# Optimization experiments

Measured on AMD Instinct MI355X. Metric: run time of the kernel, lower is better.

Reference implementation:

```python
import jax, jax.numpy as jnp
import numpy as np

B, T, D, H, DH, COUT, PRED, K, DFF = 16, 512, 512, 8, 64, 7, 96, 16, 2048
LOW_FREQ = 1
LN_EPS = 1e-5


def _next_fast_len(n):
    while True:
        m = n
        for p in (2, 3, 5):
            while m % p == 0:
                m //= p
        if m == 1:
            return n
        n += 1


def conv1d_fft(f, g, axis=1):
    # FFT cross-correlation, matching torch conv1d_fft (roll + tail slice)
    N = f.shape[axis]
    M = g.shape[axis]
    L = _next_fast_len(N + M - 1)
    Ff = jnp.fft.rfft(f, n=L, axis=axis)
    Fg = jnp.fft.rfft(g, n=L, axis=axis)
    out = jnp.fft.irfft(Ff * jnp.conj(Fg), n=L, axis=axis)
    out = jnp.roll(out, -1, axis=axis)
    return jax.lax.slice_in_dim(out, L - N, L, axis=axis)


def es_weights(sw, T_):
    alpha = jax.nn.sigmoid(sw)                       # (h,1)
    powers = jnp.arange(T_, dtype=jnp.float32)       # (T,)
    init_w = alpha ** (powers + 1.0)                 # (h,T)
    w = (1.0 - alpha) * alpha ** powers[::-1]        # (h,T)
    return init_w.T[None, :, :, None], w.T[None, :, :, None]  # (1,T,h,1)


def exponential_smoothing(values, v0, sw, aux_values=None):
    b, t, h, d = values.shape
    init_w, w = es_weights(sw, t)
    out = init_w * v0 + conv1d_fft(values, w, axis=1)
    if aux_values is not None:
        alpha = jax.nn.sigmoid(sw).reshape(1, 1, h, 1)
        aux_w = w / jnp.maximum(1.0 - alpha, 1e-6) * alpha
        out = out + conv1d_fft(aux_values, aux_w, axis=1)
    return out


def fourier_extrapolate(x, pred_len, k, low_freq=LOW_FREQ):
    b, t, d = x.shape
    x_freq = jnp.fft.rfft(x, axis=1)                 # (b, t//2+1, d)
    hi_end = x_freq.shape[1] - 1 if t % 2 == 0 else x_freq.shape[1]
    x_freq_high = x_freq[:, low_freq:hi_end]
    k_ = k if (k is not None and k < t // 2) else max(1, hi_end - low_freq)
    k_ = min(k_, x_freq_high.shape[1])
    mag = jnp.abs(x_freq_high).transpose(0, 2, 1)    # (b,d,F)
    _, idx = jax.lax.top_k(mag, k_)                  # (b,d,k)
    idx = idx.transpose(0, 2, 1) + low_freq          # (b,k,d)
    x_topk = jnp.take_along_axis(x_freq, idx, axis=1)
    freqs = jnp.fft.rfftfreq(t).astype(jnp.float32)
    f_topk = jnp.take_along_axis(
        jnp.broadcast_to(freqs[None, :, None], (b, freqs.shape[0], d)), idx, axis=1)
    x_ex = jnp.concatenate([x_topk, jnp.conj(x_topk)], axis=1)   # (b,2k,d)
    f_ex = jnp.concatenate([f_topk, -f_topk], axis=1)
    tt = jnp.arange(t + pred_len, dtype=jnp.float32)[None, None, :, None]
    amp = (jnp.abs(x_ex) / t)[:, :, None, :]
    phase = jnp.angle(x_ex)[:, :, None, :]
    x_time = amp * jnp.cos(2.0 * jnp.pi * f_ex[:, :, None, :] * tt + phase)
    return x_time.sum(axis=1)                        # (b, t+pred_len, d)


def layer_norm(x, g, b, eps=LN_EPS):
    mu = x.mean(-1, keepdims=True)
    var = ((x - mu) ** 2).mean(-1, keepdims=True)
    return (x - mu) / jnp.sqrt(var + eps) * g + b


def _forward(res, level, Wi, bi, z0, v0_g, sw_g, Wo, bo, W1, W2,
             g1, b1_ln, g2, b2_ln, Wg, bg, Ws, bs, v0_l, sw_l):
    b, t, _ = res.shape
    # season block
    season = fourier_extrapolate(res, PRED, K)               # (b, t+PRED, d)
    res1 = res - season[:, :t]
    # growth block
    v = (res1 @ Wi.T + bi).reshape(b, t, H, DH)
    v = jnp.concatenate([jnp.broadcast_to(z0[None, None], (b, 1, H, DH)), v], axis=1)
    diffs = v[:, 1:] - v[:, :-1]                             # (b,t,H,DH)
    sm = exponential_smoothing(diffs, v0_g, sw_g)
    gr = jnp.concatenate([jnp.broadcast_to(v0_g, (b, 1, H, DH)), sm], axis=1)
    growth = gr.reshape(b, t + 1, H * DH) @ Wo.T + bo        # (b,t+1,d)
    # residual path
    h = layer_norm(res1 - growth[:, 1:], g1, b1_ln)
    ff = jax.nn.relu(h @ W1.T) @ W2.T
    h = layer_norm(h + ff, g2, b2_ln)
    # level block
    gp = growth[:, 1:t + 1] @ Wg.T + bg                      # (b,t,COUT)
    sp = season[:, :t] @ Ws.T + bs
    es_in = (level - sp)[..., None]                          # (b,t,COUT,1)
    lvl = exponential_smoothing(es_in, v0_l, sw_l, aux_values=gp[..., None])[..., 0]
    return h, lvl, growth, season


def setup_inputs() -> dict:
    key = jax.random.key(0)
    ks = jax.random.split(key, 20)
    s = 0.02
    return {
        "res": jax.random.normal(ks[0], (B, T, D), jnp.float32),
        "level": jax.random.normal(ks[1], (B, T, COUT), jnp.float32),
        "Wi": jax.random.normal(ks[2], (H * DH, D), jnp.float32) * s,
        "bi": jnp.zeros((H * DH,), jnp.float32),
        "z0": jax.random.normal(ks[3], (H, DH), jnp.float32),
        "v0_g": jax.random.normal(ks[4], (1, 1, H, DH), jnp.float32),
        "sw_g": jax.random.normal(ks[5], (H, 1), jnp.float32),
        "Wo": jax.random.normal(ks[6], (D, H * DH), jnp.float32) * s,
        "bo": jnp.zeros((D,), jnp.float32),
        "W1": jax.random.normal(ks[7], (DFF, D), jnp.float32) * s,
        "W2": jax.random.normal(ks[8], (D, DFF), jnp.float32) * s,
        "g1": jnp.ones((D,), jnp.float32),
        "b1_ln": jnp.zeros((D,), jnp.float32),
        "g2": jnp.ones((D,), jnp.float32),
        "b2_ln": jnp.zeros((D,), jnp.float32),
        "Wg": jax.random.normal(ks[9], (COUT, D), jnp.float32) * s,
        "bg": jnp.zeros((COUT,), jnp.float32),
        "Ws": jax.random.normal(ks[10], (COUT, D), jnp.float32) * s,
        "bs": jnp.zeros((COUT,), jnp.float32),
        "v0_l": jax.random.normal(ks[11], (1, 1, COUT, 1), jnp.float32),
        "sw_l": jax.random.normal(ks[12], (COUT, 1), jnp.float32),
    }


def reference(res, level, Wi, bi, z0, v0_g, sw_g, Wo, bo, W1, W2,
              g1, b1_ln, g2, b2_ln, Wg, bg, Ws, bs, v0_l, sw_l):
    return _forward(res, level, Wi, bi, z0, v0_g, sw_g, Wo, bo, W1, W2,
                    g1, b1_ln, g2, b2_ln, Wg, bg, Ws, bs, v0_l, sw_l)
```

## Files before the change

kernel.cpp:

```cpp
#include <hip/hip_runtime.h>
#include <math.h>

#define Bn 16
#define Tn 512
#define Dn 512
#define COUTn 7
#define PREDn 96

using f32x4 = __attribute__((ext_vector_type(4))) float;
using bf16x8 = __attribute__((ext_vector_type(8))) __bf16;

__device__ __forceinline__ unsigned short f2b(float f) {
  unsigned int u = __float_as_uint(f);
  u += 0x7fff + ((u >> 16) & 1);
  return (unsigned short)(u >> 16);
}

__device__ __forceinline__ void gld16(const void* g, void* l) {
  __builtin_amdgcn_global_load_lds(
      (const __attribute__((address_space(1))) void*)g,
      (__attribute__((address_space(3))) void*)l, 16, 0, 0);
}

__global__ __launch_bounds__(256) void cvt_bf16(
    const float* __restrict__ in, unsigned short* __restrict__ out, int n) {
  int i = (blockIdx.x * 256 + threadIdx.x) * 4;
  if (i + 3 < n) {
    float4 v = *reinterpret_cast<const float4*>(&in[i]);
    ushort4 o;
    o.x = f2b(v.x); o.y = f2b(v.y); o.z = f2b(v.z); o.w = f2b(v.w);
    *reinterpret_cast<ushort4*>(&out[i]) = o;
  }
}

__global__ __launch_bounds__(256) void twiddle_init2(
    unsigned short* __restrict__ twc_b, unsigned short* __restrict__ tws_b,
    double* __restrict__ tabw, float* __restrict__ c512,
    float* __restrict__ s512) {
  int idx = blockIdx.x * 256 + threadIdx.x;
  int k = idx >> 9, t = idx & 511;
  int m = (k * t) & 511;
  double ang = (double)m * (M_PI / 256.0);
  twc_b[idx] = f2b((float)cos(ang));
  tws_b[idx] = f2b((float)sin(ang));
  if (idx < 512) {
    double a2 = (double)idx * (M_PI / 256.0);
    c512[idx] = (float)cos(a2);
    s512[idx] = (float)sin(a2);
    tabw[2 * idx] = cos(a2);
    tabw[2 * idx + 1] = -sin(a2);
  }
}

__global__ __launch_bounds__(256) void transpose_cvt(
    const float* __restrict__ res, unsigned short* __restrict__ resT) {
  __shared__ unsigned short tile[64][65];
  int b = blockIdx.z;
  int t0 = blockIdx.y * 64, d0 = blockIdx.x * 64;
  int tid = threadIdx.x;
  int c = tid & 63, r4 = (tid >> 6) * 16;
#pragma unroll
  for (int i = 0; i < 16; ++i) {
    int t = t0 + r4 + i;
    tile[r4 + i][c] = f2b(res[((size_t)(b * 512 + t)) * 512 + d0 + c]);
  }
  __syncthreads();
#pragma unroll
  for (int i = 0; i < 16; ++i) {
    int d = d0 + r4 + i;
    resT[((size_t)(b * 512 + d)) * 512 + t0 + c] = tile[c][r4 + i];
  }
}

__global__ __launch_bounds__(256) void screen_mfma(
    const unsigned short* __restrict__ twc_b,
    const unsigned short* __restrict__ tws_b,
    const unsigned short* __restrict__ resT, float* __restrict__ mag) {
  __shared__ unsigned short lAc[2][2048];
  __shared__ unsigned short lAs[2][2048];
  __shared__ unsigned short lB[2][4096];
  int tid = threadIdx.x;
  int wv = tid >> 6, lane = tid & 63;
  int b = blockIdx.z;
  int k0 = blockIdx.y * 64;
  int d0 = blockIdx.x * 128;

  int rA = wv * 16 + (lane >> 2);
  int rB0 = wv * 32 + (lane >> 2);
  int rB1 = rB0 + 16;
  int kk = (lane & 3) * 8;
  int kkA = kk ^ (((rA >> 1) & 3) << 3);
  int kkB0 = kk ^ (((rB0 >> 1) & 3) << 3);
  int kkB1 = kk ^ (((rB1 >> 1) & 3) << 3);
  const unsigned short* ac = twc_b + (size_t)(k0 + rA) * 512 + kkA;
  const unsigned short* as = tws_b + (size_t)(k0 + rA) * 512 + kkA;
  const unsigned short* bb0 = resT + ((size_t)(b * 512 + d0 + rB0)) * 512 + kkB0;
  const unsigned short* bb1 = resT + ((size_t)(b * 512 + d0 + rB1)) * 512 + kkB1;

  int frow = lane & 15, fk = (lane >> 4) * 8;
  int ia[4], ib[2];
#pragma unroll
  for (int i = 0; i < 4; ++i) {
    int r = i * 16 + frow;
    ia[i] = r * 32 + (fk ^ (((r >> 1) & 3) << 3));
  }
#pragma unroll
  for (int j = 0; j < 2; ++j) {
    int r = wv * 32 + j * 16 + frow;
    ib[j] = r * 32 + (fk ^ (((r >> 1) & 3) << 3));
  }

  f32x4 accR[4][2] = {};
  f32x4 accI[4][2] = {};

  gld16(ac, &lAc[0][wv * 512]);
  gld16(as, &lAs[0][wv * 512]);
  gld16(bb0, &lB[0][wv * 1024]);
  gld16(bb1, &lB[0][wv * 1024 + 512]);
  __syncthreads();

  int cur = 0;
  for (int t = 0; t < 16; ++t) {
    if (t + 1 < 16) {
      int ko = (t + 1) * 32;
      gld16(ac + ko, &lAc[cur ^ 1][wv * 512]);
      gld16(as + ko, &lAs[cur ^ 1][wv * 512]);
      gld16(bb0 + ko, &lB[cur ^ 1][wv * 1024]);
      gld16(bb1 + ko, &lB[cur ^ 1][wv * 1024 + 512]);
    }
    bf16x8 afc[4], afs[4], bw[2];
#pragma unroll
    for (int i = 0; i < 4; ++i) {
      afc[i] = *reinterpret_cast<const bf16x8*>(&lAc[cur][ia[i]]);
      afs[i] = *reinterpret_cast<const bf16x8*>(&lAs[cur][ia[i]]);
    }
#pragma unroll
    for (int j = 0; j < 2; ++j)
      bw[j] = *reinterpret_cast<const bf16x8*>(&lB[cur][ib[j]]);
#pragma unroll
    for (int i = 0; i < 4; ++i)
#pragma unroll
      for (int j = 0; j < 2; ++j) {
        accR[i][j] = __builtin_amdgcn_mfma_f32_16x16x32_bf16(
            afc[i], bw[j], accR[i][j], 0, 0, 0);
        accI[i][j] = __builtin_amdgcn_mfma_f32_16x16x32_bf16(
            afs[i], bw[j], accI[i][j], 0, 0, 0);
      }
    __syncthreads();
    cur ^= 1;
  }

  int ccol = lane & 15, crow4 = (lane >> 4) * 4;
#pragma unroll
  for (int i = 0; i < 4; ++i) {
    int kb = k0 + i * 16 + crow4;
#pragma unroll
    for (int j = 0; j < 2; ++j) {
      int d = d0 + wv * 32 + j * 16 + ccol;
#pragma unroll
      for (int r = 0; r < 4; ++r) {
        float re = accR[i][j][r], im = accI[i][j][r];
        mag[((size_t)(b * 256 + kb + r)) * 512 + d] = re * re + im * im;
      }
    }
  }
}

__global__ __launch_bounds__(64) void cand32(
    const float* __restrict__ mag, int* __restrict__ cand) {
  int blk = blockIdx.x;
  int b = blk >> 9;
  int d = blk & 511;
  int lane = threadIdx.x;
  float m2[4];
#pragma unroll
  for (int i = 0; i < 4; ++i) {
    int k = 1 + lane + 64 * i;
    m2[i] = (k <= 255) ? mag[((size_t)(b * 256 + k)) * 512 + d] : -1.f;
  }
  for (int j = 0; j < 32; ++j) {
    float bm = -2.f; int bk = 1 << 20;
#pragma unroll
    for (int i = 0; i < 4; ++i) {
      int k = 1 + lane + 64 * i;
      if (m2[i] > bm || (m2[i] == bm && k < bk)) { bm = m2[i]; bk = k; }
    }
    for (int o = 32; o > 0; o >>= 1) {
      float om = __shfl_down(bm, o, 64);
      int ok = __shfl_down(bk, o, 64);
      if (om > bm || (om == bm && ok < bk)) { bm = om; bk = ok; }
    }
    bk = __shfl(bk, 0, 64);
    if (lane == 0) cand[((size_t)(b * 32 + j)) * 512 + d] = bk;
#pragma unroll
    for (int i = 0; i < 4; ++i) {
      int k = 1 + lane + 64 * i;
      if (k == bk) m2[i] = -1.f;
    }
  }
}

__global__ __launch_bounds__(512) void refine32(
    const float* __restrict__ res, const int* __restrict__ cand,
    const double* __restrict__ tabw, int* __restrict__ kidx,
    float* __restrict__ cjb, float* __restrict__ sjb) {
  int b = blockIdx.y;
  int d0 = blockIdx.x * 16;
  int tid = threadIdx.x;
  __shared__ float colbuf[512][17];
  for (int idx = tid; idx < 8192; idx += 512) {
    int t = idx >> 4, c = idx & 15;
    colbuf[t][c] = res[((size_t)(b * 512 + t)) * 512 + d0 + c];
  }
  __syncthreads();

  int j = tid & 31, c = tid >> 5;
  int k = cand[((size_t)(b * 32 + j)) * 512 + d0 + c];
  double wr = tabw[2 * k], wi = tabw[2 * k + 1];
  double zr = 1.0, zi = 0.0, ar = 0.0, ai = 0.0;
#pragma unroll 4
  for (int t = 0; t < 512; ++t) {
    double x = (double)colbuf[t][c];
    ar = fma(x, zr, ar);
    ai = fma(x, zi, ai);
    double nzr = fma(zr, wr, -zi * wi);
    double nzi = fma(zr, wi, zi * wr);
    zr = nzr; zi = nzi;
  }
  double m2 = ar * ar + ai * ai;
  float cjv = (float)(ar * (2.0 / 512.0));
  float sjv = (float)(ai * (2.0 / 512.0));
  for (int jo = 0; jo < 16; ++jo) {
    double bm = m2; int bk = k;
#pragma unroll
    for (int o = 16; o > 0; o >>= 1) {
      double om = __shfl_xor(bm, o, 32);
      int ok = __shfl_xor(bk, o, 32);
      if (om > bm || (om == bm && ok < bk)) { bm = om; bk = ok; }
    }
    if (k == bk) {
      size_t o = ((size_t)(b * 16 + jo)) * 512 + d0 + c;
      kidx[o] = k; cjb[o] = cjv; sjb[o] = sjv;
      m2 = -1.0;
    }
  }
}

__global__ __launch_bounds__(512) void synth_kernel(
    const int* __restrict__ kidx, const float* __restrict__ cjb,
    const float* __restrict__ sjb, const float* __restrict__ c512,
    const float* __restrict__ s512, const float* __restrict__ res,
    float* __restrict__ season, unsigned short* __restrict__ res1b) {
  int b = blockIdx.y;
  int t0 = blockIdx.x * 16;
  int d = threadIdx.x;

  __shared__ float ct[512], st[512];
  ct[d] = c512[d];
  st[d] = s512[d];
  __syncthreads();

  int kk[16];
  float cw[16], sw[16];
#pragma unroll
  for (int j = 0; j < 16; ++j) {
    size_t o = ((size_t)(b * 16 + j)) * 512 + d;
    kk[j] = kidx[o];
    cw[j] = cjb[o];
    sw[j] = sjb[o];
  }

  for (int tt = 0; tt < 16; ++tt) {
    int t = t0 + tt;
    if (t >= Tn + PREDn) break;
    float acc = 0.f;
#pragma unroll
    for (int j = 0; j < 16; ++j) {
      int m = (kk[j] * t) & 511;
      acc += cw[j] * ct[m] - sw[j] * st[m];
    }
    season[((size_t)(b * (Tn + PREDn) + t)) * 512 + d] = acc;
    if (t < Tn) {
      size_t o = ((size_t)(b * Tn + t)) * 512 + d;
      res1b[o] = f2b(res[o] - acc);
    }
  }
}

template <int MODE, int BN>
__global__ __launch_bounds__(256) void gemm_mfma(
    const unsigned short* __restrict__ A, const unsigned short* __restrict__ W,
    const float* __restrict__ bias, float* __restrict__ C,
    unsigned short* __restrict__ Cb, int M, int N, int Kd, int ldk) {
  constexpr int NF = BN / 32;
  __shared__ unsigned short lA[2][4096];
  __shared__ unsigned short lB[2][BN * 32];
  int tid = threadIdx.x;
  int wv = tid >> 6, lane = tid & 63;
  int m0 = blockIdx.y * 128, n0 = blockIdx.x * BN;
  int koff = blockIdx.z * Kd;
  int wr = (wv >> 1) * 64, wc = (wv & 1) * (BN / 2);

  int rA0 = wv * 32 + (lane >> 2);
  int rA1 = rA0 + 16;
  int kk = (lane & 3) * 8;
  int kkA0 = kk ^ (((rA0 >> 1) & 3) << 3);
  int kkA1 = kk ^ (((rA1 >> 1) & 3) << 3);
  int gmA0 = m0 + rA0; if (gmA0 > M - 1) gmA0 = M - 1;
  int gmA1 = m0 + rA1; if (gmA1 > M - 1) gmA1 = M - 1;
  const unsigned short* a0 = A + (size_t)gmA0 * ldk + koff + kkA0;
  const unsigned short* a1 = A + (size_t)gmA1 * ldk + koff + kkA1;

  const unsigned short* b0;
  const unsigned short* b1 = nullptr;
  int dBo;
  if constexpr (BN == 128) {
    int rB0 = wv * 32 + (lane >> 2);
    int rB1 = rB0 + 16;
    int kkB0 = kk ^ (((rB0 >> 1) & 3) << 3);
    int kkB1 = kk ^ (((rB1 >> 1) & 3) << 3);
    b0 = W + (size_t)(n0 + rB0) * ldk + koff + kkB0;
    b1 = W + (size_t)(n0 + rB1) * ldk + koff + kkB1;
    dBo = wv * 1024;
  } else {
    int rB = wv * 16 + (lane >> 2);
    int kkB = kk ^ (((rB >> 1) & 3) << 3);
    b0 = W + (size_t)(n0 + rB) * ldk + koff + kkB;
    dBo = wv * 512;
  }

  int frow = lane & 15, fk = (lane >> 4) * 8;
  int ia[4], ib[NF];
#pragma unroll
  for (int i = 0; i < 4; ++i) {
    int r = wr + i * 16 + frow;
    ia[i] = r * 32 + (fk ^ (((r >> 1) & 3) << 3));
  }
#pragma unroll
  for (int j = 0; j < NF; ++j) {
    int r = wc + j * 16 + frow;
    ib[j] = r * 32 + (fk ^ (((r >> 1) & 3) << 3));
  }

  f32x4 acc[4][NF] = {};
  int nk = Kd >> 5;

  gld16(a0, &lA[0][wv * 1024]);
  gld16(a1, &lA[0][wv * 1024 + 512]);
  gld16(b0, &lB[0][dBo]);
  if constexpr (BN == 128) gld16(b1, &lB[0][dBo + 512]);
  __syncthreads();

  int cur = 0;
  for (int t = 0; t < nk; ++t) {
    if (t + 1 < nk) {
      int ko = (t + 1) << 5;
      gld16(a0 + ko, &lA[cur ^ 1][wv * 1024]);
      gld16(a1 + ko, &lA[cur ^ 1][wv * 1024 + 512]);
      gld16(b0 + ko, &lB[cur ^ 1][dBo]);
      if constexpr (BN == 128) gld16(b1 + ko, &lB[cur ^ 1][dBo + 512]);
    }
    bf16x8 af[4], bw[NF];
#pragma unroll
    for (int i = 0; i < 4; ++i)
      af[i] = *reinterpret_cast<const bf16x8*>(&lA[cur][ia[i]]);
#pragma unroll
    for (int j = 0; j < NF; ++j)
      bw[j] = *reinterpret_cast<const bf16x8*>(&lB[cur][ib[j]]);
#pragma unroll
    for (int i = 0; i < 4; ++i)
#pragma unroll
      for (int j = 0; j < NF; ++j)
        acc[i][j] = __builtin_amdgcn_mfma_f32_16x16x32_bf16(
            af[i], bw[j], acc[i][j], 0, 0, 0);
    __syncthreads();
    cur ^= 1;
  }

  int ccol = lane & 15, crow4 = (lane >> 4) * 4;
#pragma unroll
  for (int i = 0; i < 4; ++i) {
    int gm0 = m0 + wr + i * 16 + crow4;
#pragma unroll
    for (int j = 0; j < NF; ++j) {
      int gn = n0 + wc + j * 16 + ccol;
      float bv = 0.f;
      if (MODE == 0) bv = bias[gn];
#pragma unroll
      for (int r = 0; r < 4; ++r) {
        int gm = gm0 + r;
        if (gm < M) {
          size_t o = (size_t)gm * N + gn;
          float v = acc[i][j][r] + bv;
          if (MODE == 1) Cb[o] = f2b(fmaxf(v, 0.f));
          else if (MODE == 3) atomicAdd(&C[o], v);
          else C[o] = v;
        }
      }
    }
  }
}

__global__ __launch_bounds__(256) void ema_gA(
    const float* __restrict__ v, const float* __restrict__ z0,
    const float* __restrict__ sw_g, float* __restrict__ tmp,
    float* __restrict__ sumend) {
  int g = blockIdx.x * 256 + threadIdx.x;
  int hd = g & 511;
  int ch = (g >> 9) & 7;
  int b = g >> 12;
  int h = hd >> 6;
  float alpha = 1.f / (1.f + expf(-sw_g[h]));
  float om = 1.f - alpha;
  int t0 = ch * 64;
  float prev = (t0 == 0) ? z0[hd] : v[((size_t)(b * 512 + t0 - 1)) * 512 + hd];
  float s = 0.f;
  for (int i = 0; i < 64; ++i) {
    float cur = v[((size_t)(b * 512 + t0 + i)) * 512 + hd];
    s = alpha * s + om * (cur - prev);
    prev = cur;
    tmp[((size_t)(b * 512 + t0 + i)) * 512 + hd] = s;
  }
  sumend[((size_t)(b * 512 + hd)) * 8 + ch] = s;
}

__global__ __launch_bounds__(256) void ema_gB(
    const float* __restrict__ sumend, const float* __restrict__ v0_g,
    const float* __restrict__ sw_g, float* __restrict__ carry,
    unsigned short* __restrict__ grb) {
  int g = blockIdx.x * 256 + threadIdx.x;
  int hd = g & 511, b = g >> 9, h = hd >> 6;
  float alpha = 1.f / (1.f + expf(-sw_g[h]));
  float A64 = exp2f(64.f * log2f(alpha));
  float cin = v0_g[hd];
  grb[((size_t)(b * 513)) * 512 + hd] = f2b(cin);
  for (int ch = 0; ch < 8; ++ch) {
    carry[((size_t)(b * 512 + hd)) * 8 + ch] = cin;
    cin = A64 * cin + sumend[((size_t)(b * 512 + hd)) * 8 + ch];
  }
}

__global__ __launch_bounds__(256) void ema_gC(
    const float* __restrict__ tmp, const float* __restrict__ carry,
    const float* __restrict__ sw_g, unsigned short* __restrict__ grb) {
  int g = blockIdx.x * 256 + threadIdx.x;
  int hd = g & 511;
  int t = (g >> 9) & 511;
  int b = g >> 18;
  int h = hd >> 6;
  float alpha = 1.f / (1.f + expf(-sw_g[h]));
  int ch = t >> 6, i = t & 63;
  float Ai = exp2f((float)(i + 1) * log2f(alpha));
  float s = tmp[g] + Ai * carry[((size_t)(b * 512 + hd)) * 8 + ch];
  grb[((size_t)(b * 513 + t + 1)) * 512 + hd] = f2b(s);
}

__global__ __launch_bounds__(256) void ln0_kernel(
    const float* __restrict__ res, const float* __restrict__ season,
    const float* __restrict__ growth, const float* __restrict__ g,
    const float* __restrict__ bvec, float* __restrict__ h1,
    unsigned short* __restrict__ h1b) {
  int row = blockIdx.x, b = row >> 9, t = row & 511;
  int tid = threadIdx.x;
  const float* xr = res + (size_t)row * 512;
  const float* sr = season + ((size_t)(b * (Tn + PREDn) + t)) * 512;
  const float* gr = growth + ((size_t)(b * (Tn + 1) + t + 1)) * 512;
  float2 xv = *reinterpret_cast<const float2*>(&xr[tid * 2]);
  float2 sv = *reinterpret_cast<const float2*>(&sr[tid * 2]);
  float2 gv2 = *reinterpret_cast<const float2*>(&gr[tid * 2]);
  float v0 = xv.x - sv.x - gv2.x;
  float v1 = xv.y - sv.y - gv2.y;
  float s1 = v0 + v1;
  float s2 = v0 * v0 + v1 * v1;
  for (int o = 32; o > 0; o >>= 1) {
    s1 += __shfl_down(s1, o, 64);
    s2 += __shfl_down(s2, o, 64);
  }
  __shared__ float r1[4], r2[4];
  __shared__ float mu_s, rstd_s;
  int wv = tid >> 6, ln = tid & 63;
  if (ln == 0) { r1[wv] = s1; r2[wv] = s2; }
  __syncthreads();
  if (tid == 0) {
    float S1 = r1[0] + r1[1] + r1[2] + r1[3];
    float S2 = r2[0] + r2[1] + r2[2] + r2[3];
    float mu = S1 * (1.0f / 512.0f);
    float var = S2 * (1.0f / 512.0f) - mu * mu;
    mu_s = mu;
    rstd_s = rsqrtf(var + 1e-5f);
  }
  __syncthreads();
  float mu = mu_s, rstd = rstd_s;
  float2 gv = *reinterpret_cast<const float2*>(&g[tid * 2]);
  float2 bv = *reinterpret_cast<const float2*>(&bvec[tid * 2]);
  float o0 = (v0 - mu) * rstd * gv.x + bv.x;
  float o1 = (v1 - mu) * rstd * gv.y + bv.y;
  size_t o = (size_t)row * 512 + tid * 2;
  *reinterpret_cast<float2*>(&h1[o]) = make_float2(o0, o1);
  ushort2 hb; hb.x = f2b(o0); hb.y = f2b(o1);
  *reinterpret_cast<ushort2*>(&h1b[o]) = hb;
}

__global__ __launch_bounds__(256) void ln1_kernel(
    const float* __restrict__ X, const float* __restrict__ g,
    const float* __restrict__ bvec, float* __restrict__ out) {
  int row = blockIdx.x;
  int tid = threadIdx.x;
  const float* xr = X + (size_t)row * 512;
  float2 xv = *reinterpret_cast<const float2*>(&xr[tid * 2]);
  float v0 = xv.x, v1 = xv.y;
  float s1 = v0 + v1;
  float s2 = v0 * v0 + v1 * v1;
  for (int o = 32; o > 0; o >>= 1) {
    s1 += __shfl_down(s1, o, 64);
    s2 += __shfl_down(s2, o, 64);
  }
  __shared__ float r1[4], r2[4];
  __shared__ float mu_s, rstd_s;
  int wv = tid >> 6, ln = tid & 63;
  if (ln == 0) { r1[wv] = s1; r2[wv] = s2; }
  __syncthreads();
  if (tid == 0) {
    float S1 = r1[0] + r1[1] + r1[2] + r1[3];
    float S2 = r2[0] + r2[1] + r2[2] + r2[3];
    float mu = S1 * (1.0f / 512.0f);
    float var = S2 * (1.0f / 512.0f) - mu * mu;
    mu_s = mu;
    rstd_s = rsqrtf(var + 1e-5f);
  }
  __syncthreads();
  float mu = mu_s, rstd = rstd_s;
  float2 gv = *reinterpret_cast<const float2*>(&g[tid * 2]);
  float2 bv = *reinterpret_cast<const float2*>(&bvec[tid * 2]);
  float o0 = (v0 - mu) * rstd * gv.x + bv.x;
  float o1 = (v1 - mu) * rstd * gv.y + bv.y;
  *reinterpret_cast<float2*>(&out[(size_t)row * 512 + tid * 2]) =
      make_float2(o0, o1);
}

__global__ __launch_bounds__(64) void proj7_dual(
    const float* __restrict__ growth, const float* __restrict__ season,
    const float* __restrict__ Wg, const float* __restrict__ bg,
    const float* __restrict__ Wse, const float* __restrict__ bs,
    float* __restrict__ gpb, float* __restrict__ spb) {
  int bt = blockIdx.x;
  int which = blockIdx.y;
  int b = bt >> 9;
  int t = bt & 511;
  int lane = threadIdx.x;
  const float* X = which ? season : growth;
  int strB = which ? (Tn + PREDn) : (Tn + 1);
  int off = which ? 0 : 1;
  const float* Wc = which ? Wse : Wg;
  const float* bc = which ? bs : bg;
  float* outp = which ? spb : gpb;
  const float* row = X + ((size_t)(b * strB + off + t)) * 512;
  float x[8];
#pragma unroll
  for (int i = 0; i < 8; ++i) x[i] = row[lane + 64 * i];
#pragma unroll
  for (int c = 0; c < 7; ++c) {
    float s = 0.f;
#pragma unroll
    for (int i = 0; i < 8; ++i) s += x[i] * Wc[c * 512 + lane + 64 * i];
    for (int o = 32; o > 0; o >>= 1) s += __shfl_down(s, o, 64);
    if (lane == 0) outp[((size_t)bt) * 7 + c] = s + bc[c];
  }
}

__global__ __launch_bounds__(256) void lvl_scan(
    const float* __restrict__ level, const float* __restrict__ sp,
    const float* __restrict__ gp, const float* __restrict__ v0_l,
    const float* __restrict__ sw_l, float* __restrict__ out_lvl) {
  int blk = blockIdx.x;
  int b = blk / 7, c = blk % 7;
  int tid = threadIdx.x;
  float alpha = 1.f / (1.f + expf(-sw_l[c]));
  float om = 1.f - alpha;
  size_t i0 = ((size_t)(b * 512 + 2 * tid)) * 7 + c;
  size_t i1 = i0 + 7;
  float u0 = om * (level[i0] - sp[i0]) + alpha * gp[i0];
  float u1 = om * (level[i1] - sp[i1]) + alpha * gp[i1];
  __shared__ float As[256], Us[256];
  As[tid] = alpha * alpha;
  Us[tid] = alpha * u0 + u1;
  __syncthreads();
  for (int off = 1; off < 256; off <<= 1) {
    float Ap = 1.f, Up = 0.f;
    if (tid >= off) { Ap = As[tid - off]; Up = Us[tid - off]; }
    __syncthreads();
    if (tid >= off) {
      float Ac = As[tid], Uc = Us[tid];
      As[tid] = Ac * Ap;
      Us[tid] = Ac * Up + Uc;
    }
    __syncthreads();
  }
  float v0 = v0_l[c];
  float Aex = (tid == 0) ? 1.f : As[tid - 1];
  float Uex = (tid == 0) ? 0.f : Us[tid - 1];
  float sprev = Aex * v0 + Uex;
  float o0 = alpha * sprev + u0;
  float o1 = alpha * o0 + u1;
  out_lvl[i0] = o0;
  out_lvl[i1] = o1;
}

extern "C" void kernel_launch(void* const* d_in, const int* in_sizes, int n_in,
                              void* d_out, int out_size, void* d_ws,
                              size_t ws_size, hipStream_t stream) {
  const float* res = (const float*)d_in[0];
  const float* level = (const float*)d_in[1];
  const float* Wi = (const float*)d_in[2];
  const float* bi = (const float*)d_in[3];
  const float* z0 = (const float*)d_in[4];
  const float* v0_g = (const float*)d_in[5];
  const float* sw_g = (const float*)d_in[6];
  const float* Wo = (const float*)d_in[7];
  const float* bo = (const float*)d_in[8];
  const float* W1 = (const float*)d_in[9];
  const float* W2 = (const float*)d_in[10];
  const float* g1 = (const float*)d_in[11];
  const float* b1 = (const float*)d_in[12];
  const float* g2 = (const float*)d_in[13];
  const float* b2 = (const float*)d_in[14];
  const float* Wg = (const float*)d_in[15];
  const float* bg = (const float*)d_in[16];
  const float* Wse = (const float*)d_in[17];
  const float* bs = (const float*)d_in[18];
  const float* v0_l = (const float*)d_in[19];
  const float* sw_l = (const float*)d_in[20];

  float* out = (float*)d_out;
  float* out_h = out;
  float* out_lvl = out + 4194304;
  float* out_growth = out + 4251648;
  float* out_season = out + 8454144;

  float* wsf = (float*)d_ws;
  unsigned short* res1_b = (unsigned short*)wsf;
  unsigned short* h1_b = (unsigned short*)wsf;
  float* gpb = wsf;
  float* spb = wsf + 57344;
  unsigned short* resT_b = (unsigned short*)(wsf + 2097152);
  float* magb = wsf + 4194304;
  int* candb = (int*)(wsf + 6291456);
  unsigned short* twc_b = (unsigned short*)(wsf + 6553600);
  unsigned short* tws_b = (unsigned short*)(wsf + 6619136);
  float* vbuf = wsf + 2097152;
  unsigned short* grbuf_b = (unsigned short*)(wsf + 6291456);
  float* sumend = wsf + 8392704;
  float* carryb = wsf + 8458240;
  unsigned short* ff1_b = (unsigned short*)(wsf + 2097152);
  double* tabw = (double*)(wsf + 10485760);
  float* c512 = wsf + 10487808;
  float* s512 = wsf + 10488320;
  int* kidx = (int*)(wsf + 10488832);
  float* cjb = wsf + 10619904;
  float* sjb = wsf + 10750976;
  float* tmpb = wsf + 10485760;
  float* h1 = wsf + 10485760;
  unsigned short* Wi_b = (unsigned short*)(wsf + 14680064);
  unsigned short* Wo_b = (unsigned short*)(wsf + 14811136);
  unsigned short* W1_b = (unsigned short*)(wsf + 14942208);
  unsigned short* W2_b = (unsigned short*)(wsf + 15466496);

  hipLaunchKernelGGL(cvt_bf16, dim3(256), dim3(256), 0, stream, Wi, Wi_b, 262144);
  hipLaunchKernelGGL(cvt_bf16, dim3(256), dim3(256), 0, stream, Wo, Wo_b, 262144);
  hipLaunchKernelGGL(cvt_bf16, dim3(1024), dim3(256), 0, stream, W1, W1_b, 1048576);
  hipLaunchKernelGGL(cvt_bf16, dim3(1024), dim3(256), 0, stream, W2, W2_b, 1048576);

  hipLaunchKernelGGL(twiddle_init2, dim3(512), dim3(256), 0, stream,
                     twc_b, tws_b, tabw, c512, s512);
  hipLaunchKernelGGL(transpose_cvt, dim3(8, 8, 16), dim3(256), 0, stream,
                     res, resT_b);
  hipLaunchKernelGGL(screen_mfma, dim3(4, 4, 16), dim3(256), 0, stream,
                     twc_b, tws_b, resT_b, magb);
  hipLaunchKernelGGL(cand32, dim3(8192), dim3(64), 0, stream, magb, candb);
  hipLaunchKernelGGL(refine32, dim3(32, 16), dim3(512), 0, stream,
                     res, candb, tabw, kidx, cjb, sjb);
  hipLaunchKernelGGL(synth_kernel, dim3(38, 16), dim3(512), 0, stream,
                     kidx, cjb, sjb, c512, s512, res, out_season, res1_b);
  hipLaunchKernelGGL((gemm_mfma<0, 64>), dim3(8, 64, 1), dim3(256), 0, stream,
                     res1_b, Wi_b, bi, vbuf, (unsigned short*)nullptr,
                     8192, 512, 512, 512);
  hipLaunchKernelGGL(ema_gA, dim3(256), dim3(256), 0, stream,
                     vbuf, z0, sw_g, tmpb, sumend);
  hipLaunchKernelGGL(ema_gB, dim3(32), dim3(256), 0, stream,
                     sumend, v0_g, sw_g, carryb, grbuf_b);
  hipLaunchKernelGGL(ema_gC, dim3(16384), dim3(256), 0, stream,
                     tmpb, carryb, sw_g, grbuf_b);
  hipLaunchKernelGGL((gemm_mfma<0, 64>), dim3(8, 65, 1), dim3(256), 0, stream,
                     grbuf_b, Wo_b, bo, out_growth, (unsigned short*)nullptr,
                     8208, 512, 512, 512);
  hipLaunchKernelGGL(ln0_kernel, dim3(Bn * Tn), dim3(256), 0, stream,
                     res, out_season, out_growth, g1, b1, h1, h1_b);
  hipLaunchKernelGGL((gemm_mfma<1, 128>), dim3(16, 64, 1), dim3(256), 0, stream,
                     h1_b, W1_b, (const float*)nullptr, (float*)nullptr, ff1_b,
                     8192, 2048, 512, 512);
  hipLaunchKernelGGL((gemm_mfma<3, 64>), dim3(8, 64, 4), dim3(256), 0, stream,
                     ff1_b, W2_b, (const float*)nullptr, h1,
                     (unsigned short*)nullptr, 8192, 512, 512, 2048);
  hipLaunchKernelGGL(ln1_kernel, dim3(Bn * Tn), dim3(256), 0, stream,
                     h1, g2, b2, out_h);
  hipLaunchKernelGGL(proj7_dual, dim3(Bn * Tn, 2), dim3(64), 0, stream,
                     out_growth, out_season, Wg, bg, Wse, bs, gpb, spb);
  hipLaunchKernelGGL(lvl_scan, dim3(112), dim3(256), 0, stream,
                     level, spb, gpb, v0_l, sw_l, out_lvl);

  (void)in_sizes; (void)n_in; (void)out_size; (void)ws_size;
}
```

Measured before the change: 506.9 us.

## Generalize GEMM tiles to 64x128, swap grid axes, replace split-K atomics with two passes

The MFMA GEMM is templated on both tile dimensions and all four projections now use 64x128 tiles. The grid is reordered so blockIdx.x walks M, which changes how blocks share weight tiles in cache. The FFN down-projection drops the 4-way split-K with atomicAdd and instead runs two sequential launches over K halves that add into the residual with plain read-modify-write. This removes atomic traffic but adds a launch, halves the parallelism of the W2 GEMM, and changes tile occupancy for every GEMM.

Result: faster. 481.4 us (-5.0%).

```diff
diff --git a/kernel.cpp b/kernel.cpp
--- a/kernel.cpp
+++ b/kernel.cpp
@@ -287,52 +287,44 @@
   }
 }
 
-template <int MODE, int BN>
+template <int MODE, int BM, int BN>
 __global__ __launch_bounds__(256) void gemm_mfma(
     const unsigned short* __restrict__ A, const unsigned short* __restrict__ W,
     const float* __restrict__ bias, float* __restrict__ C,
-    unsigned short* __restrict__ Cb, int M, int N, int Kd, int ldk) {
+    unsigned short* __restrict__ Cb, int M, int N, int Kd, int ldk,
+    int k0off) {
+  constexpr int MF = BM / 32;
   constexpr int NF = BN / 32;
-  __shared__ unsigned short lA[2][4096];
+  constexpr int NSA = BM / 64;
+  constexpr int NSB = BN / 64;
+  __shared__ unsigned short lA[2][BM * 32];
   __shared__ unsigned short lB[2][BN * 32];
   int tid = threadIdx.x;
   int wv = tid >> 6, lane = tid & 63;
-  int m0 = blockIdx.y * 128, n0 = blockIdx.x * BN;
-  int koff = blockIdx.z * Kd;
-  int wr = (wv >> 1) * 64, wc = (wv & 1) * (BN / 2);
-
-  int rA0 = wv * 32 + (lane >> 2);
-  int rA1 = rA0 + 16;
+  int m0 = blockIdx.x * BM, n0 = blockIdx.y * BN;
+  int wr = (wv >> 1) * (BM / 2), wc = (wv & 1) * (BN / 2);
   int kk = (lane & 3) * 8;
-  int kkA0 = kk ^ (((rA0 >> 1) & 3) << 3);
-  int kkA1 = kk ^ (((rA1 >> 1) & 3) << 3);
-  int gmA0 = m0 + rA0; if (gmA0 > M - 1) gmA0 = M - 1;
-  int gmA1 = m0 + rA1; if (gmA1 > M - 1) gmA1 = M - 1;
-  const unsigned short* a0 = A + (size_t)gmA0 * ldk + koff + kkA0;
-  const unsigned short* a1 = A + (size_t)gmA1 * ldk + koff + kkA1;
-
-  const unsigned short* b0;
-  const unsigned short* b1 = nullptr;
-  int dBo;
-  if constexpr (BN == 128) {
-    int rB0 = wv * 32 + (lane >> 2);
-    int rB1 = rB0 + 16;
-    int kkB0 = kk ^ (((rB0 >> 1) & 3) << 3);
-    int kkB1 = kk ^ (((rB1 >> 1) & 3) << 3);
-    b0 = W + (size_t)(n0 + rB0) * ldk + koff + kkB0;
-    b1 = W + (size_t)(n0 + rB1) * ldk + koff + kkB1;
-    dBo = wv * 1024;
-  } else {
-    int rB = wv * 16 + (lane >> 2);
-    int kkB = kk ^ (((rB >> 1) & 3) << 3);
-    b0 = W + (size_t)(n0 + rB) * ldk + koff + kkB;
-    dBo = wv * 512;
+
+  const unsigned short* aptr[NSA];
+  const unsigned short* bptr[NSB];
+#pragma unroll
+  for (int g = 0; g < NSA; ++g) {
+    int rA = wv * (BM / 4) + g * 16 + (lane >> 2);
+    int kkg = kk ^ (((rA >> 1) & 3) << 3);
+    int gm = m0 + rA; if (gm > M - 1) gm = M - 1;
+    aptr[g] = A + (size_t)gm * ldk + k0off + kkg;
+  }
+#pragma unroll
+  for (int g = 0; g < NSB; ++g) {
+    int rB = wv * (BN / 4) + g * 16 + (lane >> 2);
+    int kkg = kk ^ (((rB >> 1) & 3) << 3);
+    bptr[g] = W + (size_t)(n0 + rB) * ldk + k0off + kkg;
   }
 
   int frow = lane & 15, fk = (lane >> 4) * 8;
-  int ia[4], ib[NF];
-#pragma unroll
-  for (int i = 0; i < 4; ++i) {
+  int ia[MF], ib[NF];
+#pragma unroll
+  for (int i = 0; i < MF; ++i) {
     int r = wr + i * 16 + frow;
     ia[i] = r * 32 + (fk ^ (((r >> 1) & 3) << 3));
   }
@@ -342,33 +334,35 @@
     ib[j] = r * 32 + (fk ^ (((r >> 1) & 3) << 3));
   }
 
-  f32x4 acc[4][NF] = {};
+  f32x4 acc[MF][NF] = {};
   int nk = Kd >> 5;
 
-  gld16(a0, &lA[0][wv * 1024]);
-  gld16(a1, &lA[0][wv * 1024 + 512]);
-  gld16(b0, &lB[0][dBo]);
-  if constexpr (BN == 128) gld16(b1, &lB[0][dBo + 512]);
+#pragma unroll
+  for (int g = 0; g < NSA; ++g) gld16(aptr[g], &lA[0][wv * BM * 8 + g * 512]);
+#pragma unroll
+  for (int g = 0; g < NSB; ++g) gld16(bptr[g], &lB[0][wv * BN * 8 + g * 512]);
   __syncthreads();
 
   int cur = 0;
   for (int t = 0; t < nk; ++t) {
     if (t + 1 < nk) {
       int ko = (t + 1) << 5;
-      gld16(a0 + ko, &lA[cur ^ 1][wv * 1024]);
-      gld16(a1 + ko, &lA[cur ^ 1][wv * 1024 + 512]);
-      gld16(b0 + ko, &lB[cur ^ 1][dBo]);
-      if constexpr (BN == 128) gld16(b1 + ko, &lB[cur ^ 1][dBo + 512]);
-    }
-    bf16x8 af[4], bw[NF];
-#pragma unroll
-    for (int i = 0; i < 4; ++i)
+#pragma unroll
+      for (int g = 0; g < NSA; ++g)
+        gld16(aptr[g] + ko, &lA[cur ^ 1][wv * BM * 8 + g * 512]);
+#pragma unroll
+      for (int g = 0; g < NSB; ++g)
+        gld16(bptr[g] + ko, &lB[cur ^ 1][wv * BN * 8 + g * 512]);
+    }
+    bf16x8 af[MF], bw[NF];
+#pragma unroll
+    for (int i = 0; i < MF; ++i)
       af[i] = *reinterpret_cast<const bf16x8*>(&lA[cur][ia[i]]);
 #pragma unroll
     for (int j = 0; j < NF; ++j)
       bw[j] = *reinterpret_cast<const bf16x8*>(&lB[cur][ib[j]]);
 #pragma unroll
-    for (int i = 0; i < 4; ++i)
+    for (int i = 0; i < MF; ++i)
 #pragma unroll
       for (int j = 0; j < NF; ++j)
         acc[i][j] = __builtin_amdgcn_mfma_f32_16x16x32_bf16(
@@ -379,7 +373,7 @@
 
   int ccol = lane & 15, crow4 = (lane >> 4) * 4;
 #pragma unroll
-  for (int i = 0; i < 4; ++i) {
+  for (int i = 0; i < MF; ++i) {
     int gm0 = m0 + wr + i * 16 + crow4;
 #pragma unroll
     for (int j = 0; j < NF; ++j) {
@@ -393,7 +387,7 @@
           size_t o = (size_t)gm * N + gn;
           float v = acc[i][j][r] + bv;
           if (MODE == 1) Cb[o] = f2b(fmaxf(v, 0.f));
-          else if (MODE == 3) atomicAdd(&C[o], v);
+          else if (MODE == 2) C[o] += v;
           else C[o] = v;
         }
       }
@@ -681,26 +675,29 @@
                      res, candb, tabw, kidx, cjb, sjb);
   hipLaunchKernelGGL(synth_kernel, dim3(38, 16), dim3(512), 0, stream,
                      kidx, cjb, sjb, c512, s512, res, out_season, res1_b);
-  hipLaunchKernelGGL((gemm_mfma<0, 64>), dim3(8, 64, 1), dim3(256), 0, stream,
-                     res1_b, Wi_b, bi, vbuf, (unsigned short*)nullptr,
-                     8192, 512, 512, 512);
+  hipLaunchKernelGGL((gemm_mfma<0, 64, 128>), dim3(128, 4), dim3(256), 0,
+                     stream, res1_b, Wi_b, bi, vbuf, (unsigned short*)nullptr,
+                     8192, 512, 512, 512, 0);
   hipLaunchKernelGGL(ema_gA, dim3(256), dim3(256), 0, stream,
                      vbuf, z0, sw_g, tmpb, sumend);
   hipLaunchKernelGGL(ema_gB, dim3(32), dim3(256), 0, stream,
                      sumend, v0_g, sw_g, carryb, grbuf_b);
   hipLaunchKernelGGL(ema_gC, dim3(16384), dim3(256), 0, stream,
                      tmpb, carryb, sw_g, grbuf_b);
-  hipLaunchKernelGGL((gemm_mfma<0, 64>), dim3(8, 65, 1), dim3(256), 0, stream,
-                     grbuf_b, Wo_b, bo, out_growth, (unsigned short*)nullptr,
-                     8208, 512, 512, 512);
+  hipLaunchKernelGGL((gemm_mfma<0, 64, 128>), dim3(129, 4), dim3(256), 0,
+                     stream, grbuf_b, Wo_b, bo, out_growth,
+                     (unsigned short*)nullptr, 8208, 512, 512, 512, 0);
   hipLaunchKernelGGL(ln0_kernel, dim3(Bn * Tn), dim3(256), 0, stream,
                      res, out_season, out_growth, g1, b1, h1, h1_b);
-  hipLaunchKernelGGL((gemm_mfma<1, 128>), dim3(16, 64, 1), dim3(256), 0, stream,
-                     h1_b, W1_b, (const float*)nullptr, (float*)nullptr, ff1_b,
-                     8192, 2048, 512, 512);
-  hipLaunchKernelGGL((gemm_mfma<3, 64>), dim3(8, 64, 4), dim3(256), 0, stream,
-                     ff1_b, W2_b, (const float*)nullptr, h1,
-                     (unsigned short*)nullptr, 8192, 512, 512, 2048);
+  hipLaunchKernelGGL((gemm_mfma<1, 64, 128>), dim3(128, 16), dim3(256), 0,
+                     stream, h1_b, W1_b, (const float*)nullptr,
+                     (float*)nullptr, ff1_b, 8192, 2048, 512, 512, 0);
+  hipLaunchKernelGGL((gemm_mfma<2, 64, 128>), dim3(128, 4), dim3(256), 0,
+                     stream, ff1_b, W2_b, (const float*)nullptr, h1,
+                     (unsigned short*)nullptr, 8192, 512, 1024, 2048, 0);
+  hipLaunchKernelGGL((gemm_mfma<2, 64, 128>), dim3(128, 4), dim3(256), 0,
+                     stream, ff1_b, W2_b, (const float*)nullptr, h1,
+                     (unsigned short*)nullptr, 8192, 512, 1024, 2048, 1024);
   hipLaunchKernelGGL(ln1_kernel, dim3(Bn * Tn), dim3(256), 0, stream,
                      h1, g2, b2, out_h);
   hipLaunchKernelGGL(proj7_dual, dim3(Bn * Tn, 2), dim3(64), 0, stream,
```
